# Kernel optimization log

Hardware: AMD Instinct MI355X
Metric: run time of the kernel (lower is better)

The kernel has to match this reference:

```python
import jax, jax.numpy as jnp
import numpy as np

SIDE_LEN = 128
RESOLUTION = 1.0  # Angstrom per pixel


def setup_inputs() -> dict:
    key = jax.random.key(0)
    k1, k2, k3 = jax.random.split(key, 3)
    B, A = 16, 20000
    # atom xyz coords in Angstrom, spread within the field of view (+/- 63.5 A)
    mol = jax.random.normal(k1, (B, A, 3), dtype=jnp.float32) * 20.0
    # per-atom Gaussian std in [0.5, 1.5) A (strictly positive)
    stds = jax.random.uniform(k2, (A,), dtype=jnp.float32) + 0.5
    # per-atom density (mass) in [0.5, 1.5)
    densities = jax.random.uniform(k3, (A,), dtype=jnp.float32) + 0.5
    return {"mol": mol, "stds": stds, "densities": densities}


def reference(mol, stds, densities):
    # Pixel-center coordinate grid, identical to torch.arange(-x_max, x_max+1e-5, res)
    x_max = (SIDE_LEN - 1) * RESOLUTION / 2
    coord = jnp.arange(-x_max, x_max + 1e-5, RESOLUTION, dtype=jnp.float32)  # (S,)
    var = stds * stds                              # (A,)
    neg_half_inv_var = (-0.5 / var)[None, :, None] # (1,A,1)
    # Separable Gaussian profiles: exp(-(coord - mu)^2 / (2 var))
    dx = coord[None, None, :] - mol[:, :, 0:1]     # (B,A,S) x-offsets
    dy = coord[None, None, :] - mol[:, :, 1:2]     # (B,A,S) y-offsets
    gx = jnp.exp(neg_half_inv_var * dx * dx)       # (B,A,W)
    gy = jnp.exp(neg_half_inv_var * dy * dy)       # (B,A,H)
    coef = densities / (2.0 * jnp.pi * var)        # (A,)
    # img[b,h,w] = sum_a coef_a * gy[b,a,h] * gx[b,a,w]  (batched matmul)
    img = jnp.einsum('bah,baw->bhw', gy * coef[None, :, None], gx)
    return img  # (B, SIDE_LEN, SIDE_LEN)
```

## Files before the change

### kernel.cpp

```cpp
#include <hip/hip_runtime.h>


#define S 128
#define NS 32
#define PER 640
#define BLOCK 512

typedef _Float16 f16;
typedef _Float16 f16x2 __attribute__((ext_vector_type(2)));
typedef _Float16 f16x8 __attribute__((ext_vector_type(8)));
typedef float floatx16 __attribute__((ext_vector_type(16)));

#if __has_builtin(__builtin_amdgcn_exp2f)
#define FAST_EXP2(x) __builtin_amdgcn_exp2f(x)
#else
#define FAST_EXP2(x) exp2f(x)
#endif
#if __has_builtin(__builtin_amdgcn_rcpf)
#define FAST_RCP(x) __builtin_amdgcn_rcpf(x)
#else
#define FAST_RCP(x) (1.0f / (x))
#endif

static __device__ __forceinline__ f16x2 PKRTZ(float a, float b) {
#if __has_builtin(__builtin_amdgcn_cvt_pkrtz)
    return __builtin_bit_cast(f16x2, __builtin_amdgcn_cvt_pkrtz(a, b));
#else
    return (f16x2){(f16)a, (f16)b};
#endif
}

union frag_u { f16x8 v; f16x2 h[4]; };

__global__ __launch_bounds__(BLOCK, 4) void k_proj(
    const float* __restrict__ mol,
    const float* __restrict__ stds,
    const float* __restrict__ dens,
    f16* __restrict__ part,
    int B, int A)
{
    __shared__ float4 sP[PER];
    __shared__ float red[4 * 4096];

    const int ks   = blockIdx.x;
    const int b    = blockIdx.y;
    const int tid  = threadIdx.x;
    const int lane = tid & 63;
    const int wav  = tid >> 6;
    const int quad = wav & 3;
    const int half = wav >> 2;
    const int l31  = lane & 31;
    const int hi   = lane >> 5;

    const int a0  = ks * PER;
    const int a1  = min(a0 + PER, A);
    const int cnt = a1 - a0;

    for (int i = tid; i < cnt; i += BLOCK) {
        const int a = a0 + i;
        const size_t idx = (size_t)b * A + a;
        float x  = mol[idx * 3 + 0];
        float y  = mol[idx * 3 + 1];
        float v  = stds[a] * stds[a];
        float rv = FAST_RCP(v);
        sP[i] = make_float4(x, y, -0.72134752044448f * rv,
                            __log2f(dens[a] * 0.15915494309189535f * rv));
    }
    __syncthreads();

    const int hcnt = cnt >> 1;
    const int nk   = hcnt >> 4;

    const float py0 = (float)((quad >> 1) * 64 + l31) - 63.5f;
    const float px0 = (float)((quad & 1) * 64 + l31) - 63.5f;

    floatx16 acc[2][2];
#pragma unroll
    for (int rr = 0; rr < 2; ++rr)
#pragma unroll
        for (int cb = 0; cb < 2; ++cb) acc[rr][cb] = (floatx16){0.f};

    const float4* sp = sP + half * hcnt + hi * 8;

    for (int s = 0; s < nk; ++s) {
        const float4* pp = sp + (size_t)s * 16;
        frag_u A0, A1, B0, B1;
#pragma unroll
        for (int jp = 0; jp < 4; ++jp) {
            float ea0[2], ea1[2], eb0[2], eb1[2];
#pragma unroll
            for (int u = 0; u < 2; ++u) {
                float4 p = pp[2 * jp + u];
                float dy = py0 - p.y;
                float t  = p.z * dy;
                float g0 = fmaf(t, dy, p.w);
                float g1 = fmaf(1024.0f, p.z, fmaf(64.0f, t, g0));
                ea0[u] = FAST_EXP2(g0);
                ea1[u] = FAST_EXP2(g1);
                float dx = px0 - p.x;
                float sx = p.z * dx;
                float h0 = sx * dx;
                float h1 = fmaf(1024.0f, p.z, fmaf(64.0f, sx, h0));
                eb0[u] = FAST_EXP2(h0);
                eb1[u] = FAST_EXP2(h1);
            }
            A0.h[jp] = PKRTZ(ea0[0], ea0[1]);
            A1.h[jp] = PKRTZ(ea1[0], ea1[1]);
            B0.h[jp] = PKRTZ(eb0[0], eb0[1]);
            B1.h[jp] = PKRTZ(eb1[0], eb1[1]);
        }
        acc[0][0] = __builtin_amdgcn_mfma_f32_32x32x16_f16(A0.v, B0.v, acc[0][0], 0, 0, 0);
        acc[0][1] = __builtin_amdgcn_mfma_f32_32x32x16_f16(A0.v, B1.v, acc[0][1], 0, 0, 0);
        acc[1][0] = __builtin_amdgcn_mfma_f32_32x32x16_f16(A1.v, B0.v, acc[1][0], 0, 0, 0);
        acc[1][1] = __builtin_amdgcn_mfma_f32_32x32x16_f16(A1.v, B1.v, acc[1][1], 0, 0, 0);
    }

    float* rq = red + quad * 4096;
    if (half == 0) {
#pragma unroll
        for (int rr = 0; rr < 2; ++rr)
#pragma unroll
            for (int cb = 0; cb < 2; ++cb) {
                float* t = rq + (rr * 2 + cb) * 1024 + lane;
#pragma unroll
                for (int j = 0; j < 16; ++j) t[j * 64] = acc[rr][cb][j];
            }
    }
    __syncthreads();

    if (half == 1) {
        f16* base = part + ((size_t)(b * NS + ks)) * (S * S) + lane * 16;
#pragma unroll
        for (int rr = 0; rr < 2; ++rr)
#pragma unroll
            for (int cb = 0; cb < 2; ++cb) {
                float* t = rq + (rr * 2 + cb) * 1024 + lane;
                floatx16 v = acc[rr][cb];
#pragma unroll
                for (int j = 0; j < 16; ++j) v[j] += t[j * 64];
                const int tileidx = ((quad >> 1) * 2 + rr) * 4 + ((quad & 1) * 2 + cb);
                f16* pq = base + (size_t)tileidx * 1024;
                frag_u lo, hiv;
#pragma unroll
                for (int jp = 0; jp < 4; ++jp) {
                    lo.h[jp]  = PKRTZ(v[2 * jp],     v[2 * jp + 1]);
                    hiv.h[jp] = PKRTZ(v[2 * jp + 8], v[2 * jp + 9]);
                }
                *(f16x8*)(pq + 0) = lo.v;
                *(f16x8*)(pq + 8) = hiv.v;
            }
    }
}

__global__ __launch_bounds__(256) void k_reduce(const f16* __restrict__ part,
                                                float* __restrict__ out) {
    const int b  = blockIdx.z;
    const int f8 = (blockIdx.x * 256 + threadIdx.x) * 8;

    const f16* src = part + (size_t)b * NS * (S * S) + f8;
    float s0[8] = {0.f}, s1[8] = {0.f};
    for (int s = 0; s < NS; s += 2) {
        f16x8 v0 = *(const f16x8*)&src[(size_t)s * (S * S)];
        f16x8 v1 = *(const f16x8*)&src[(size_t)(s + 1) * (S * S)];
#pragma unroll
        for (int i = 0; i < 8; ++i) { s0[i] += (float)v0[i]; s1[i] += (float)v1[i]; }
    }

    const int reg0 = f8 & 15;
    const int lane = (f8 >> 4) & 63;
    const int tile = f8 >> 10;
    const int r    = tile >> 2;
    const int cc   = tile & 3;
    const int rowb = r * 32 + 4 * (lane >> 5);
    const int col  = cc * 32 + (lane & 31);
#pragma unroll
    for (int i = 0; i < 8; ++i) {
        const int reg = reg0 + i;
        const int row = rowb + (reg & 3) + 8 * (reg >> 2);
        out[((size_t)b * S + row) * S + col] = s0[i] + s1[i];
    }
}

extern "C" void kernel_launch(void* const* d_in, const int* in_sizes, int n_in,
                              void* d_out, int out_size, void* d_ws, size_t ws_size,
                              hipStream_t stream) {
    const float* mol  = (const float*)d_in[0];
    const float* stds = (const float*)d_in[1];
    const float* dens = (const float*)d_in[2];
    float* out = (float*)d_out;

    const int A = in_sizes[1];
    const int B = in_sizes[0] / (A * 3);

    f16* part = (f16*)d_ws;

    k_proj<<<dim3(NS, B), dim3(BLOCK), 0, stream>>>(mol, stds, dens, part, B, A);
    k_reduce<<<dim3((S * S) / (256 * 8), 1, B), dim3(256), 0, stream>>>(part, out);
}
```

Baseline: 93.54 us.

## Replace partial-buffer reduce kernel with float atomicAdd into zeroed output

```diff
diff --git a/kernel.cpp b/kernel.cpp
--- a/kernel.cpp
+++ b/kernel.cpp
@@ -36,7 +36,7 @@
     const float* __restrict__ mol,
     const float* __restrict__ stds,
     const float* __restrict__ dens,
-    f16* __restrict__ part,
+    float* __restrict__ out,
     int B, int A)
 {
     __shared__ float4 sP[PER];
@@ -129,7 +129,9 @@
     __syncthreads();
 
     if (half == 1) {
-        f16* base = part + ((size_t)(b * NS + ks)) * (S * S) + lane * 16;
+        float* ob = out + (size_t)b * S * S;
+        const int rowq = (quad >> 1) * 64 + 4 * hi;
+        const int colq = (quad & 1) * 64 + l31;
 #pragma unroll
         for (int rr = 0; rr < 2; ++rr)
 #pragma unroll
@@ -138,46 +140,14 @@
                 floatx16 v = acc[rr][cb];
 #pragma unroll
                 for (int j = 0; j < 16; ++j) v[j] += t[j * 64];
-                const int tileidx = ((quad >> 1) * 2 + rr) * 4 + ((quad & 1) * 2 + cb);
-                f16* pq = base + (size_t)tileidx * 1024;
-                frag_u lo, hiv;
+                const int row0 = rowq + rr * 32;
+                const int col  = colq + cb * 32;
 #pragma unroll
-                for (int jp = 0; jp < 4; ++jp) {
-                    lo.h[jp]  = PKRTZ(v[2 * jp],     v[2 * jp + 1]);
-                    hiv.h[jp] = PKRTZ(v[2 * jp + 8], v[2 * jp + 9]);
+                for (int j = 0; j < 16; ++j) {
+                    const int row = row0 + (j & 3) + 8 * (j >> 2);
+                    atomicAdd(&ob[(size_t)row * S + col], v[j]);
                 }
-                *(f16x8*)(pq + 0) = lo.v;
-                *(f16x8*)(pq + 8) = hiv.v;
             }
-    }
-}
-
-__global__ __launch_bounds__(256) void k_reduce(const f16* __restrict__ part,
-                                                float* __restrict__ out) {
-    const int b  = blockIdx.z;
-    const int f8 = (blockIdx.x * 256 + threadIdx.x) * 8;
-
-    const f16* src = part + (size_t)b * NS * (S * S) + f8;
-    float s0[8] = {0.f}, s1[8] = {0.f};
-    for (int s = 0; s < NS; s += 2) {
-        f16x8 v0 = *(const f16x8*)&src[(size_t)s * (S * S)];
-        f16x8 v1 = *(const f16x8*)&src[(size_t)(s + 1) * (S * S)];
-#pragma unroll
-        for (int i = 0; i < 8; ++i) { s0[i] += (float)v0[i]; s1[i] += (float)v1[i]; }
-    }
-
-    const int reg0 = f8 & 15;
-    const int lane = (f8 >> 4) & 63;
-    const int tile = f8 >> 10;
-    const int r    = tile >> 2;
-    const int cc   = tile & 3;
-    const int rowb = r * 32 + 4 * (lane >> 5);
-    const int col  = cc * 32 + (lane & 31);
-#pragma unroll
-    for (int i = 0; i < 8; ++i) {
-        const int reg = reg0 + i;
-        const int row = rowb + (reg & 3) + 8 * (reg >> 2);
-        out[((size_t)b * S + row) * S + col] = s0[i] + s1[i];
     }
 }
 
@@ -192,8 +162,6 @@
     const int A = in_sizes[1];
     const int B = in_sizes[0] / (A * 3);
 
-    f16* part = (f16*)d_ws;
-
-    k_proj<<<dim3(NS, B), dim3(BLOCK), 0, stream>>>(mol, stds, dens, part, B, A);
-    k_reduce<<<dim3((S * S) / (256 * 8), 1, B), dim3(256), 0, stream>>>(part, out);
+    hipMemsetAsync(d_out, 0, (size_t)out_size * sizeof(float), stream);
+    k_proj<<<dim3(NS, B), dim3(BLOCK), 0, stream>>>(mol, stds, dens, out, B, A);
 }
```

After: 99.69 us. 1.07x slower.
